# Performance work log

Hardware: AMD Instinct MI355X
Metric: run time of the kernel (lower is better)

The kernel has to match this reference:

```python
import jax, jax.numpy as jnp
import numpy as np

MAX_SHIFT = 1          # max_shift_size
COS_EPS = 1e-8         # torch F.cosine_similarity default eps
EPSILON = 1e-16        # sharpening denominator epsilon


def setup_inputs() -> dict:
    key = jax.random.key(0)
    ks = jax.random.split(key, 7)
    B, N, D = 64, 4096, 256
    return {
        "m": jax.random.normal(ks[0], (B, N, D), dtype=jnp.float32),
        "k": jax.random.normal(ks[1], (B, D), dtype=jnp.float32),
        "b": jax.random.uniform(ks[2], (B, 1), dtype=jnp.float32),
        "g": jax.random.uniform(ks[3], (B, 1), dtype=jnp.float32),
        "s": jax.random.uniform(ks[4], (B, 2 * MAX_SHIFT + 1), dtype=jnp.float32),
        "r": jax.random.uniform(ks[5], (B, 1), dtype=jnp.float32),
        "w_prev": jax.random.uniform(ks[6], (B, N), dtype=jnp.float32),
    }


def reference(m, k, b, g, s, r, w_prev):
    # --- content addressing: softmax(b * cosine_sim(m, k)) over memory slots ---
    dot = jnp.einsum("bnd,bd->bn", m, k)                      # [B, N]
    m_norm = jnp.maximum(jnp.linalg.norm(m, axis=-1), COS_EPS)  # [B, N]
    k_norm = jnp.maximum(jnp.linalg.norm(k, axis=-1), COS_EPS)  # [B]
    cos = dot / (m_norm * k_norm[:, None])
    w = jax.nn.softmax(b * cos, axis=1)                       # [B, N]
    # --- interpolate with current (previous) position ---
    w = w + (1.0 - g) * w_prev
    # --- circular shift (direct gather of shifted windows, O(B*N*(2S+1))) ---
    N = w.shape[1]
    wu = jnp.concatenate([w[:, -MAX_SHIFT:], w, w[:, :MAX_SHIFT]], axis=1)  # [B, N+2S]
    windows = jnp.stack([wu[:, t:t + N] for t in range(2 * MAX_SHIFT + 1)], axis=1)  # [B, 2S+1, N]
    w = jnp.einsum("bt,btn->bn", s, windows)
    # --- sharpen ---
    wr = w ** r                                               # r broadcasts [B,1]
    return wr / (jnp.sum(wr, axis=1, keepdims=True) + EPSILON)
```

## Files before the change

kernel.cpp:

```cpp
#include <hip/hip_runtime.h>
#include <math.h>

#define DDIM 256
#define NSLOT 4096
#define LOG2_NSLOT 12
#define WAVES_PER_BLOCK 4
#define ROWS_PER_BLOCK 32

typedef float f32x4 __attribute__((ext_vector_type(4)));

__global__ __launch_bounds__(256) void ntm_score_kernel(
    const float* __restrict__ m, const float* __restrict__ k,
    const float* __restrict__ beta, float* __restrict__ scores) {
  const int wave = threadIdx.x >> 6;
  const int lane = threadIdx.x & 63;
  const int grp  = lane >> 3;
  const int l    = lane & 7;
  const long long row =
      (long long)blockIdx.x * ROWS_PER_BLOCK + wave * 8 + grp;
  const int b = (int)(row >> LOG2_NSLOT);

  const float* mrow = m + row * DDIM;
  const float* krow = k + (long long)b * DDIM;

  float dot = 0.f, mm = 0.f, kk = 0.f;
  #pragma unroll
  for (int j = 0; j < 8; ++j) {
    const int off = j * 32 + l * 4;
    const f32x4 mv = *reinterpret_cast<const f32x4*>(mrow + off);
    const f32x4 kv = *reinterpret_cast<const f32x4*>(krow + off);
    dot += mv.x * kv.x + mv.y * kv.y + mv.z * kv.z + mv.w * kv.w;
    mm  += mv.x * mv.x + mv.y * mv.y + mv.z * mv.z + mv.w * mv.w;
    kk  += kv.x * kv.x + kv.y * kv.y + kv.z * kv.z + kv.w * kv.w;
  }

  #pragma unroll
  for (int off = 4; off > 0; off >>= 1) {
    dot += __shfl_xor(dot, off);
    mm  += __shfl_xor(mm, off);
    kk  += __shfl_xor(kk, off);
  }

  if (l == 0) {
    const float mn = fmaxf(sqrtf(mm), 1e-8f);
    const float kn = fmaxf(sqrtf(kk), 1e-8f);
    scores[row] = beta[b] * (dot / (mn * kn));
  }
}

__global__ __launch_bounds__(1024) void ntm_finish_kernel(
    const float* __restrict__ scores, const float* __restrict__ g,
    const float* __restrict__ s, const float* __restrict__ r,
    const float* __restrict__ w_prev, float* __restrict__ out) {
  const int b = blockIdx.x;
  const int tid = threadIdx.x;
  const int wave = tid >> 6;
  const int lane = tid & 63;

  __shared__ float  w_sh[NSLOT];
  __shared__ float  redf[16];
  __shared__ double redd[16];
  __shared__ float  bcast_f;
  __shared__ double bcast_d;

  const float* sc = scores + (size_t)b * NSLOT;
  const float* wp = w_prev + (size_t)b * NSLOT;

  float e[4];
  float mx = -INFINITY;
  #pragma unroll
  for (int i = 0; i < 4; ++i) {
    e[i] = sc[tid + i * 1024];
    mx = fmaxf(mx, e[i]);
  }
  #pragma unroll
  for (int off = 32; off > 0; off >>= 1) mx = fmaxf(mx, __shfl_xor(mx, off));
  if (lane == 0) redf[wave] = mx;
  __syncthreads();
  if (tid == 0) {
    float v = redf[0];
    #pragma unroll
    for (int i = 1; i < 16; ++i) v = fmaxf(v, redf[i]);
    bcast_f = v;
  }
  __syncthreads();
  mx = bcast_f;

  double dsum = 0.0;
  #pragma unroll
  for (int i = 0; i < 4; ++i) {
    e[i] = expf(e[i] - mx);
    dsum += (double)e[i];
  }
  #pragma unroll
  for (int off = 32; off > 0; off >>= 1) dsum += __shfl_xor(dsum, off);
  if (lane == 0) redd[wave] = dsum;
  __syncthreads();
  if (tid == 0) {
    double v = 0.0;
    #pragma unroll
    for (int i = 0; i < 16; ++i) v += redd[i];
    bcast_d = v;
  }
  __syncthreads();
  const double inv_sum = 1.0 / bcast_d;

  const float gm1 = 1.0f - g[b];
  #pragma unroll
  for (int i = 0; i < 4; ++i) {
    const int n = tid + i * 1024;
    w_sh[n] = (float)((double)e[i] * inv_sum) + gm1 * wp[n];
  }
  __syncthreads();

  const float s0 = s[b * 3 + 0];
  const float s1 = s[b * 3 + 1];
  const float s2 = s[b * 3 + 2];
  const float rv = r[b];

  float p[4];
  double psum = 0.0;
  #pragma unroll
  for (int i = 0; i < 4; ++i) {
    const int n = tid + i * 1024;
    const float left  = w_sh[(n + NSLOT - 1) & (NSLOT - 1)];
    const float mid   = w_sh[n];
    const float right = w_sh[(n + 1) & (NSLOT - 1)];
    const float v = s0 * left + s1 * mid + s2 * right;
    p[i] = powf(v, rv);
    psum += (double)p[i];
  }
  #pragma unroll
  for (int off = 32; off > 0; off >>= 1) psum += __shfl_xor(psum, off);
  if (lane == 0) redd[wave] = psum;
  __syncthreads();
  if (tid == 0) {
    double v = 1e-16;
    #pragma unroll
    for (int i = 0; i < 16; ++i) v += redd[i];
    bcast_d = v;
  }
  __syncthreads();
  const double inv_p = 1.0 / bcast_d;

  float* o = out + (size_t)b * NSLOT;
  #pragma unroll
  for (int i = 0; i < 4; ++i) {
    o[tid + i * 1024] = (float)((double)p[i] * inv_p);
  }
}

extern "C" void kernel_launch(void* const* d_in, const int* in_sizes, int n_in,
                              void* d_out, int out_size, void* d_ws, size_t ws_size,
                              hipStream_t stream) {
  const float* m      = (const float*)d_in[0];
  const float* k      = (const float*)d_in[1];
  const float* beta   = (const float*)d_in[2];
  const float* g      = (const float*)d_in[3];
  const float* s      = (const float*)d_in[4];
  const float* r      = (const float*)d_in[5];
  const float* w_prev = (const float*)d_in[6];
  float* out = (float*)d_out;
  float* scores = (float*)d_ws;

  const int B = in_sizes[1] / DDIM;
  const int rows = B * NSLOT;

  ntm_score_kernel<<<rows / ROWS_PER_BLOCK, 256, 0, stream>>>(m, k, beta, scores);
  ntm_finish_kernel<<<B, 1024, 0, stream>>>(scores, g, s, r, w_prev, out);
}
```

Baseline: 51.03 us.

## Fuse exp and softmax row-sum into score kernel via atomic per-batch sums

Measured after the change: 72.30 us. +41.7%, slower.

```diff
diff --git a/kernel.cpp b/kernel.cpp
--- a/kernel.cpp
+++ b/kernel.cpp
@@ -4,16 +4,17 @@
 #define DDIM 256
 #define NSLOT 4096
 #define LOG2_NSLOT 12
-#define WAVES_PER_BLOCK 4
 #define ROWS_PER_BLOCK 32
 
 typedef float f32x4 __attribute__((ext_vector_type(4)));
 
 __global__ __launch_bounds__(256) void ntm_score_kernel(
     const float* __restrict__ m, const float* __restrict__ k,
-    const float* __restrict__ beta, float* __restrict__ scores) {
-  const int wave = threadIdx.x >> 6;
-  const int lane = threadIdx.x & 63;
+    const float* __restrict__ beta, float* __restrict__ escores,
+    double* __restrict__ bsums) {
+  const int tid  = threadIdx.x;
+  const int wave = tid >> 6;
+  const int lane = tid & 63;
   const int grp  = lane >> 3;
   const int l    = lane & 7;
   const long long row =
@@ -41,75 +42,50 @@
     kk  += __shfl_xor(kk, off);
   }
 
-  if (l == 0) {
-    const float mn = fmaxf(sqrtf(mm), 1e-8f);
-    const float kn = fmaxf(sqrtf(kk), 1e-8f);
-    scores[row] = beta[b] * (dot / (mn * kn));
+  const float mn = fmaxf(sqrtf(mm), 1e-8f);
+  const float kn = fmaxf(sqrtf(kk), 1e-8f);
+  const float e  = expf(beta[b] * (dot / (mn * kn)));
+  if (l == 0) escores[row] = e;
+
+  double de = (double)e;
+  de += __shfl_xor(de, 8);
+  de += __shfl_xor(de, 16);
+  de += __shfl_xor(de, 32);
+
+  __shared__ double wsum[4];
+  if (lane == 0) wsum[wave] = de;
+  __syncthreads();
+  if (tid == 0) {
+    const double blocksum = wsum[0] + wsum[1] + wsum[2] + wsum[3];
+    __hip_atomic_fetch_add(&bsums[b], blocksum, __ATOMIC_RELAXED,
+                           __HIP_MEMORY_SCOPE_AGENT);
   }
 }
 
 __global__ __launch_bounds__(1024) void ntm_finish_kernel(
-    const float* __restrict__ scores, const float* __restrict__ g,
-    const float* __restrict__ s, const float* __restrict__ r,
-    const float* __restrict__ w_prev, float* __restrict__ out) {
+    const float* __restrict__ escores, const double* __restrict__ bsums,
+    const float* __restrict__ g, const float* __restrict__ s,
+    const float* __restrict__ r, const float* __restrict__ w_prev,
+    float* __restrict__ out) {
   const int b = blockIdx.x;
   const int tid = threadIdx.x;
   const int wave = tid >> 6;
   const int lane = tid & 63;
 
   __shared__ float  w_sh[NSLOT];
-  __shared__ float  redf[16];
   __shared__ double redd[16];
-  __shared__ float  bcast_f;
   __shared__ double bcast_d;
 
-  const float* sc = scores + (size_t)b * NSLOT;
+  const float* sc = escores + (size_t)b * NSLOT;
   const float* wp = w_prev + (size_t)b * NSLOT;
 
-  float e[4];
-  float mx = -INFINITY;
-  #pragma unroll
-  for (int i = 0; i < 4; ++i) {
-    e[i] = sc[tid + i * 1024];
-    mx = fmaxf(mx, e[i]);
-  }
-  #pragma unroll
-  for (int off = 32; off > 0; off >>= 1) mx = fmaxf(mx, __shfl_xor(mx, off));
-  if (lane == 0) redf[wave] = mx;
-  __syncthreads();
-  if (tid == 0) {
-    float v = redf[0];
-    #pragma unroll
-    for (int i = 1; i < 16; ++i) v = fmaxf(v, redf[i]);
-    bcast_f = v;
-  }
-  __syncthreads();
-  mx = bcast_f;
+  const double inv_sum = 1.0 / bsums[b];
+  const float gm1 = 1.0f - g[b];
 
-  double dsum = 0.0;
-  #pragma unroll
-  for (int i = 0; i < 4; ++i) {
-    e[i] = expf(e[i] - mx);
-    dsum += (double)e[i];
-  }
-  #pragma unroll
-  for (int off = 32; off > 0; off >>= 1) dsum += __shfl_xor(dsum, off);
-  if (lane == 0) redd[wave] = dsum;
-  __syncthreads();
-  if (tid == 0) {
-    double v = 0.0;
-    #pragma unroll
-    for (int i = 0; i < 16; ++i) v += redd[i];
-    bcast_d = v;
-  }
-  __syncthreads();
-  const double inv_sum = 1.0 / bcast_d;
-
-  const float gm1 = 1.0f - g[b];
   #pragma unroll
   for (int i = 0; i < 4; ++i) {
     const int n = tid + i * 1024;
-    w_sh[n] = (float)((double)e[i] * inv_sum) + gm1 * wp[n];
+    w_sh[n] = (float)((double)sc[n] * inv_sum) + gm1 * wp[n];
   }
   __syncthreads();
 
@@ -161,11 +137,17 @@
   const float* r      = (const float*)d_in[5];
   const float* w_prev = (const float*)d_in[6];
   float* out = (float*)d_out;
-  float* scores = (float*)d_ws;
 
   const int B = in_sizes[1] / DDIM;
   const int rows = B * NSLOT;
 
-  ntm_score_kernel<<<rows / ROWS_PER_BLOCK, 256, 0, stream>>>(m, k, beta, scores);
-  ntm_finish_kernel<<<B, 1024, 0, stream>>>(scores, g, s, r, w_prev, out);
+  float*  escores = (float*)d_ws;
+  double* bsums   = (double*)((char*)d_ws + (size_t)rows * sizeof(float));
+
+  hipMemsetAsync(bsums, 0, B * sizeof(double), stream);
+
+  ntm_score_kernel<<<rows / ROWS_PER_BLOCK, 256, 0, stream>>>(
+      m, k, beta, escores, bsums);
+  ntm_finish_kernel<<<B, 1024, 0, stream>>>(
+      escores, bsums, g, s, r, w_prev, out);
 }
```
